# Kernel tuning notes

Hardware: AMD Instinct MI355X
Metric: run time of the kernel (lower is better)

The kernel has to match this reference:

```python
import jax, jax.numpy as jnp
import numpy as np

B, T, HID = 2, 2048, 2048
H, KVH, D = 16, 4, 128


def _rope_tables(t, d):
    inv_freq = 1.0 / (10000.0 ** (np.arange(0, d, 2, dtype=np.float32) / d))
    freqs = np.arange(t, dtype=np.float32)[:, None] * inv_freq[None, :]  # [T, d/2]
    emb = np.concatenate([freqs, freqs], axis=-1)  # [T, d]
    return jnp.asarray(np.cos(emb))[None], jnp.asarray(np.sin(emb))[None]  # [1,T,d]


def setup_inputs() -> dict:
    key = jax.random.key(0)
    ks = jax.random.split(key, 5)
    x = jax.random.normal(ks[0], (B, T, HID), dtype=jnp.float32)
    rope_cos, rope_sin = _rope_tables(T, D)
    s_in = 1.0 / np.sqrt(HID)
    Wq = jax.random.normal(ks[1], (HID, H * D), dtype=jnp.float32) * s_in
    Wk = jax.random.normal(ks[2], (HID, KVH * D), dtype=jnp.float32) * s_in
    Wv = jax.random.normal(ks[3], (HID, KVH * D), dtype=jnp.float32) * s_in
    Wo = jax.random.normal(ks[4], (H * D, HID), dtype=jnp.float32) * (1.0 / np.sqrt(H * D))
    return {"x": x, "rope_cos": rope_cos, "rope_sin": rope_sin,
            "Wq": Wq, "Wk": Wk, "Wv": Wv, "Wo": Wo}


def _apply_rope(t, cos, sin):
    # t: [B,T,h,D]; cos/sin: [1,T,D] -> broadcast over heads
    c = cos[:, :, None, :]
    s = sin[:, :, None, :]
    t1, t2 = jnp.split(t, 2, axis=-1)
    rot = jnp.concatenate([-t2, t1], axis=-1)
    return t * c + rot * s


def reference(x, rope_cos, rope_sin, Wq, Wk, Wv, Wo):
    Tq = x.shape[1]
    q = (x @ Wq).reshape(B, Tq, H, D)
    k = (x @ Wk).reshape(B, Tq, KVH, D)
    v = (x @ Wv).reshape(B, Tq, KVH, D)
    q = _apply_rope(q, rope_cos[:, :Tq], rope_sin[:, :Tq])
    k = _apply_rope(k, rope_cos[:, :Tq], rope_sin[:, :Tq])
    # sliding_window == T -> T <= W branch: k/v unchanged
    rep = H // KVH  # GQA repeat-kv
    k_full = jnp.repeat(k, rep, axis=2)  # [B,T,H,D]
    v_full = jnp.repeat(v, rep, axis=2)
    scale = 1.0 / jnp.sqrt(jnp.asarray(D, dtype=x.dtype))
    scores = jnp.einsum('bqhd,bkhd->bhqk', q, k_full) * scale
    causal = jnp.tril(jnp.ones((Tq, Tq), dtype=bool))  # end-aligned, Tk==Tq
    scores = jnp.where(causal[None, None], scores, jnp.asarray(-jnp.inf, scores.dtype))
    p = jax.nn.softmax(scores, axis=-1)
    out = jnp.einsum('bhqk,bkhd->bqhd', p, v_full)
    return out.reshape(B, Tq, H * D) @ Wo
```

## Files before the change

### kernel.cpp

```cpp
#include <hip/hip_runtime.h>
#include <hip/hip_bf16.h>

#define B_   2
#define T_   2048
#define HID_ 2048
#define H_   16
#define KVH_ 4
#define D_   128
#define GQ_  (H_ / KVH_)

#define QN_  8388608
#define KN_  2097152

typedef unsigned short u16;
typedef __attribute__((ext_vector_type(8))) unsigned short us8v;
typedef __attribute__((ext_vector_type(8))) short s16x8;
typedef __attribute__((ext_vector_type(4))) float f32x4;

__device__ __forceinline__ float bf2f(u16 u) {
  return __uint_as_float(((unsigned)u) << 16);
}
__device__ __forceinline__ u16 f2bf(float f) {
  unsigned x = __float_as_uint(f);
  return (u16)((x + 0x7fffu + ((x >> 16) & 1u)) >> 16);
}

__device__ __forceinline__ void gl2lds(const void* gp, void* lp) {
  __builtin_amdgcn_global_load_lds(
      (const __attribute__((address_space(1))) unsigned int*)gp,
      (__attribute__((address_space(3))) unsigned int*)lp, 16, 0, 0);
}

__device__ __forceinline__ void probe2(const void* A, const void* W, int tid,
                                       bool* abf, bool* wbf) {
  __shared__ int cA, zA, cW, zW;
  if (tid == 0) { cA = 0; zA = 0; cW = 0; zW = 0; }
  __syncthreads();
  const int i = 16384 + tid;
  {
    const u16 raw = ((const u16*)A)[i];
    const float v = bf2f(raw);
    const bool bad = !(fabsf(v) <= 1e6f) ||
                     (v != 0.0f && fabsf(v) < 1e-10f);
    if (bad) atomicAdd(&cA, 1);
    if (((tid & 1) == 0) && raw == 0) atomicAdd(&zA, 1);
  }
  {
    const u16 raw = ((const u16*)W)[i];
    const float v = bf2f(raw);
    const bool bad = !(fabsf(v) <= 1e6f) ||
                     (v != 0.0f && fabsf(v) < 1e-10f);
    if (bad) atomicAdd(&cW, 1);
    if (((tid & 1) == 0) && raw == 0) atomicAdd(&zW, 1);
  }
  __syncthreads();
  *abf = (cA < 8) && (zA < 100);
  *wbf = (cW < 8) && (zW < 100);
}

__global__ __launch_bounds__(256) void transp_k(const void* __restrict__ Wv_,
                                                u16* __restrict__ WT,
                                                int K, int N) {
  const int tid = threadIdx.x;
  bool wbf, dummy;
  probe2(Wv_, Wv_, tid, &wbf, &dummy);

  __shared__ float tile[64][65];
  const int kb = blockIdx.y * 64;
  const int nb = blockIdx.x * 64;

  for (int it = tid; it < 512; it += 256) {
    const int r = it >> 3;
    const int g = it & 7;
    const size_t off = (size_t)(kb + r) * N + nb + g * 8;
    float f[8];
    if (wbf) {
      const us8v t8 = *(const us8v*)((const u16*)Wv_ + off);
#pragma unroll
      for (int e = 0; e < 8; ++e) f[e] = bf2f(t8[e]);
    } else {
      const float4 f0 = *(const float4*)((const float*)Wv_ + off);
      const float4 f1 = *(const float4*)((const float*)Wv_ + off + 4);
      f[0] = f0.x; f[1] = f0.y; f[2] = f0.z; f[3] = f0.w;
      f[4] = f1.x; f[5] = f1.y; f[6] = f1.z; f[7] = f1.w;
    }
#pragma unroll
    for (int e = 0; e < 8; ++e) tile[r][g * 8 + e] = f[e];
  }
  __syncthreads();
  for (int it = tid; it < 512; it += 256) {
    const int n = it >> 3;
    const int g = it & 7;
    us8v tmp;
#pragma unroll
    for (int e = 0; e < 8; ++e) tmp[e] = f2bf(tile[g * 8 + e][n]);
    *(us8v*)&WT[(size_t)(nb + n) * K + kb + g * 8] = tmp;
  }
}

template <int OMODE>
__global__ __launch_bounds__(256) void gemm_mfma(const void* __restrict__ Av,
                                                 const u16* __restrict__ WT,
                                                 void* __restrict__ Cv,
                                                 int M, int N, int K) {
  const int tid = threadIdx.x;
  bool abf, dummy;
  probe2(Av, Av, tid, &abf, &dummy);

  __shared__ __align__(16) u16 Alds[128 * 32];
  __shared__ __align__(16) u16 Blds[128 * 32];

  const int m0 = blockIdx.y * 128;
  const int n0 = blockIdx.x * 128;
  const int wave = tid >> 6;
  const int lane = tid & 63;
  const int wm = (wave >> 1) * 64;
  const int wn = (wave & 1) * 64;
  const int lrow = lane & 15;
  const int lq = lane >> 4;

  f32x4 acc[4][4] = {};

  for (int k0 = 0; k0 < K; k0 += 32) {
    __syncthreads();
    if (abf) {
#pragma unroll
      for (int p = 0; p < 2; ++p) {
        const int it = tid + p * 256;
        const int r = it >> 2, g = it & 3;
        const int gs = g ^ ((r >> 1) & 3);
        gl2lds((const u16*)Av + (size_t)(m0 + r) * K + k0 + gs * 8,
               &Alds[((tid & ~63) + p * 256) * 8]);
      }
    } else {
#pragma unroll
      for (int p = 0; p < 2; ++p) {
        const int it = tid + p * 256;
        const int r = it >> 2, g = it & 3;
        const int gs = g ^ ((r >> 1) & 3);
        const size_t off = (size_t)(m0 + r) * K + k0 + gs * 8;
        const float4 f0 = *(const float4*)((const float*)Av + off);
        const float4 f1 = *(const float4*)((const float*)Av + off + 4);
        us8v tmp;
        tmp[0] = f2bf(f0.x); tmp[1] = f2bf(f0.y);
        tmp[2] = f2bf(f0.z); tmp[3] = f2bf(f0.w);
        tmp[4] = f2bf(f1.x); tmp[5] = f2bf(f1.y);
        tmp[6] = f2bf(f1.z); tmp[7] = f2bf(f1.w);
        *(us8v*)&Alds[r * 32 + g * 8] = tmp;
      }
    }
#pragma unroll
    for (int p = 0; p < 2; ++p) {
      const int it = tid + p * 256;
      const int n = it >> 2, g = it & 3;
      const int gs = g ^ ((n >> 1) & 3);
      gl2lds(WT + (size_t)(n0 + n) * K + k0 + gs * 8,
             &Blds[((tid & ~63) + p * 256) * 8]);
    }
    __syncthreads();

    s16x8 af[4], bfr[4];
#pragma unroll
    for (int mi = 0; mi < 4; ++mi) {
      const int row = wm + 16 * mi + lrow;
      af[mi] = *(const s16x8*)&Alds[row * 32 + ((lq ^ ((row >> 1) & 3)) * 8)];
    }
#pragma unroll
    for (int ni = 0; ni < 4; ++ni) {
      const int row = wn + 16 * ni + lrow;
      bfr[ni] = *(const s16x8*)&Blds[row * 32 + ((lq ^ ((row >> 1) & 3)) * 8)];
    }
#pragma unroll
    for (int mi = 0; mi < 4; ++mi)
#pragma unroll
      for (int ni = 0; ni < 4; ++ni)
        acc[mi][ni] = __builtin_amdgcn_mfma_f32_16x16x32_bf16(
            af[mi], bfr[ni], acc[mi][ni], 0, 0, 0);
  }

#pragma unroll
  for (int mi = 0; mi < 4; ++mi) {
#pragma unroll
    for (int ni = 0; ni < 4; ++ni) {
      const int row0 = m0 + wm + 16 * mi + lq * 4;
      const int col = n0 + wn + 16 * ni + lrow;
#pragma unroll
      for (int r = 0; r < 4; ++r) {
        const int row = row0 + r;
        if (OMODE == 0) {
          ((float*)Cv)[(size_t)row * N + col] = acc[mi][ni][r];
        } else {
          const u16 val = f2bf(acc[mi][ni][r]);
          if (col < 2048) {
            ((u16*)Cv)[(size_t)row * 2048 + col] = val;
          } else if (col < 2560) {
            ((u16*)Cv)[QN_ + (size_t)row * 512 + (col - 2048)] = val;
          } else {
            const int c = col - 2560;
            const int kvh = c >> 7;
            const int d = c & 127;
            const int bb = row >> 11;
            const int tt = row & (T_ - 1);
            ((u16*)Cv)[QN_ + KN_ +
                       ((size_t)(bb * KVH_ + kvh) * D_ + d) * T_ + tt] = val;
          }
        }
      }
    }
  }
}

__global__ __launch_bounds__(256) void rope_bf(u16* __restrict__ t,
                                               const void* __restrict__ cosT,
                                               const void* __restrict__ sinT,
                                               int NH, int total, float qs) {
  const int tid = threadIdx.x;
  bool cbf, sbf;
  probe2(cosT, sinT, tid, &cbf, &sbf);

  const int idx = blockIdx.x * blockDim.x + tid;
  if (idx >= total) return;
  const int d = idx & 63;
  const int rest = idx >> 6;
  const int tt = (rest / NH) % T_;
  const size_t base = (size_t)rest * D_;
  const int ci = tt * D_ + d;
  float c1, s1, c2, s2;
  if (cbf) {
    c1 = bf2f(((const u16*)cosT)[ci]);
    c2 = bf2f(((const u16*)cosT)[ci + 64]);
  } else {
    c1 = ((const float*)cosT)[ci];
    c2 = ((const float*)cosT)[ci + 64];
  }
  if (sbf) {
    s1 = bf2f(((const u16*)sinT)[ci]);
    s2 = bf2f(((const u16*)sinT)[ci + 64]);
  } else {
    s1 = ((const float*)sinT)[ci];
    s2 = ((const float*)sinT)[ci + 64];
  }
  const float x1 = bf2f(t[base + d]);
  const float x2 = bf2f(t[base + d + 64]);
  t[base + d] = f2bf((x1 * c1 - x2 * s1) * qs);
  t[base + d + 64] = f2bf((x2 * c2 + x1 * s2) * qs);
}

#define ATT_STAGE(bi, ktile)                                                  \
  do {                                                                        \
    const int _k0 = (ktile) * 64;                                             \
    u16* _bk = &SM[(bi) * 16384];                                             \
    _Pragma("unroll") for (int _p = 0; _p < 2; ++_p) {                        \
      const int _it = tid + _p * 512;                                         \
      const int _r = _it >> 4, _s = _it & 15;                                 \
      gl2lds(kp + (size_t)(_k0 + _r) * (KVH_ * D_) + ((_s ^ (_r & 7)) * 8),   \
             &_bk[((tid & ~63) + _p * 512) * 8]);                             \
    }                                                                         \
    _Pragma("unroll") for (int _p = 0; _p < 2; ++_p) {                        \
      const int _it = tid + _p * 512;                                         \
      const int _r = _it >> 3, _s = _it & 7;                                  \
      gl2lds(vp + (size_t)_r * T_ + _k0 + ((_s ^ (_r & 7)) * 8),              \
             &_bk[8192 + ((tid & ~63) + _p * 512) * 8]);                      \
    }                                                                         \
  } while (0)

__global__ __launch_bounds__(512, 4) void attn_mfma(
    const u16* __restrict__ q, const u16* __restrict__ k,
    const u16* __restrict__ vT, u16* __restrict__ o) {
  const int tid = threadIdx.x;
  const int ip = blockIdx.y;
  const int bh = blockIdx.x;
  const int b = bh >> 4;
  const int h = bh & 15;
  const int kvh = h >> 2;
  const int hi0 = 64 * (31 - ip);
  const int lo0 = 64 * ip;

  __shared__ __align__(16) u16 SM[2 * 16384];
  __shared__ __align__(16) u16 Pl[128 * 64];

  const int wave = tid >> 6;
  const int lane = tid & 63;
  const int l15 = lane & 15;
  const int quad = lane >> 4;
  const bool isHi = wave < 4;
  const int rowbase = isHi ? (hi0 + 16 * wave) : (lo0 + 16 * (wave - 4));
  const int pr0 = 16 * wave;

  const u16* kp = k + ((size_t)b * T_ * KVH_ + kvh) * D_;
  const u16* vp = vT + (size_t)(b * KVH_ + kvh) * D_ * T_;

  s16x8 qf[4];
  {
    const size_t qrow = ((size_t)(b * T_ + rowbase + l15) * H_ + h) * D_;
#pragma unroll
    for (int st = 0; st < 4; ++st)
      qf[st] = *(const s16x8*)&q[qrow + st * 32 + quad * 8];
  }

  f32x4 acc_o[8] = {};
  float m_s = -1.0e30f, l_s = 0.0f;

  const int nkt = 32 - ip;

  ATT_STAGE(0, 0);
  __syncthreads();

  for (int kt = 0; kt < nkt; ++kt) {
    const int k0 = kt * 64;
    const u16* Ks = &SM[(kt & 1) * 16384];
    const u16* Vt = Ks + 8192;

    if (kt + 1 < nkt) ATT_STAGE((kt + 1) & 1, kt + 1);

    const bool active = isHi || (kt <= ip);
    if (active) {
      f32x4 accs[4] = {};
      __builtin_amdgcn_s_setprio(1);
#pragma unroll
      for (int st = 0; st < 4; ++st) {
        const int g = st * 4 + quad;
#pragma unroll
        for (int nt = 0; nt < 4; ++nt) {
          const int row = nt * 16 + l15;
          const s16x8 kf =
              *(const s16x8*)&Ks[row * 128 + ((g ^ (row & 7)) << 3)];
          accs[nt] = __builtin_amdgcn_mfma_f32_16x16x32_bf16(kf, qf[st],
                                                             accs[nt], 0, 0,
                                                             0);
        }
      }
      __builtin_amdgcn_s_setprio(0);

      if ((k0 + 63) > rowbase) {
        const int qg = rowbase + l15;
#pragma unroll
        for (int nt = 0; nt < 4; ++nt)
#pragma unroll
          for (int r = 0; r < 4; ++r)
            if (qg < (k0 + nt * 16 + quad * 4 + r)) accs[nt][r] = -1.0e30f;
      }

      float t0 = fmaxf(fmaxf(accs[0][0], accs[0][1]),
                       fmaxf(accs[0][2], accs[0][3]));
      float t1 = fmaxf(fmaxf(accs[1][0], accs[1][1]),
                       fmaxf(accs[1][2], accs[1][3]));
      float t2 = fmaxf(fmaxf(accs[2][0], accs[2][1]),
                       fmaxf(accs[2][2], accs[2][3]));
      float t3 = fmaxf(fmaxf(accs[3][0], accs[3][1]),
                       fmaxf(accs[3][2], accs[3][3]));
      float mx = fmaxf(fmaxf(t0, t1), fmaxf(t2, t3));
      mx = fmaxf(mx, __shfl_xor(mx, 16));
      mx = fmaxf(mx, __shfl_xor(mx, 32));

      const int defer = __all(mx <= m_s + 8.0f);
      float alv = 1.0f;
      if (!defer) {
        const float mnew = fmaxf(m_s, mx);
        alv = __expf(m_s - mnew);
        m_s = mnew;
      }

#pragma unroll
      for (int nt = 0; nt < 4; ++nt)
#pragma unroll
        for (int r = 0; r < 4; ++r)
          accs[nt][r] = __expf(accs[nt][r] - m_s);

#pragma unroll
      for (int nt = 0; nt < 4; ++nt) {
        uint2 w;
        asm("v_cvt_pk_bf16_f32 %0, %1, %2"
            : "=v"(w.x) : "v"(accs[nt][0]), "v"(accs[nt][1]));
        asm("v_cvt_pk_bf16_f32 %0, %1, %2"
            : "=v"(w.y) : "v"(accs[nt][2]), "v"(accs[nt][3]));
        const int prow = pr0 + l15;
        const int c0 = nt * 16 + quad * 4;
        *(uint2*)&Pl[prow * 64 + (((c0 >> 3) ^ (prow & 7)) << 3) + (c0 & 7)] =
            w;
      }

      float s0 = (accs[0][0] + accs[0][1]) + (accs[0][2] + accs[0][3]);
      float s1 = (accs[1][0] + accs[1][1]) + (accs[1][2] + accs[1][3]);
      float s2 = (accs[2][0] + accs[2][1]) + (accs[2][2] + accs[2][3]);
      float s3 = (accs[3][0] + accs[3][1]) + (accs[3][2] + accs[3][3]);
      float rs = (s0 + s1) + (s2 + s3);
      rs += __shfl_xor(rs, 16);
      rs += __shfl_xor(rs, 32);
      l_s = l_s * alv + rs;

      if (!defer) {
#pragma unroll
        for (int r = 0; r < 4; ++r) {
          const float a4 = __shfl(alv, 4 * quad + r);
#pragma unroll
          for (int nt2 = 0; nt2 < 8; ++nt2) acc_o[nt2][r] *= a4;
        }
      }

      asm volatile("s_waitcnt lgkmcnt(0)" ::: "memory");
      __builtin_amdgcn_sched_barrier(0);

      s16x8 pa[2];
#pragma unroll
      for (int ks = 0; ks < 2; ++ks) {
        const int row = pr0 + l15;
        const int g = ks * 4 + quad;
        pa[ks] = *(const s16x8*)&Pl[row * 64 + ((g ^ (row & 7)) << 3)];
      }
      __builtin_amdgcn_s_setprio(1);
#pragma unroll
      for (int ks = 0; ks < 2; ++ks) {
        const int g = ks * 4 + quad;
#pragma unroll
        for (int nt2 = 0; nt2 < 8; ++nt2) {
          const int row = nt2 * 16 + l15;
          const s16x8 vf =
              *(const s16x8*)&Vt[row * 64 + ((g ^ (row & 7)) << 3)];
          acc_o[nt2] = __builtin_amdgcn_mfma_f32_16x16x32_bf16(pa[ks], vf,
                                                               acc_o[nt2], 0,
                                                               0, 0);
        }
      }
      __builtin_amdgcn_s_setprio(0);
    }

    __syncthreads();
  }

  const float inv = 1.0f / l_s;
#pragma unroll
  for (int r = 0; r < 4; ++r) {
    const float linv = __shfl(inv, 4 * quad + r);
    const size_t orow =
        ((size_t)(b * T_ + rowbase + quad * 4 + r) * H_ + h) * D_;
#pragma unroll
    for (int nt2 = 0; nt2 < 8; ++nt2)
      o[orow + nt2 * 16 + l15] = f2bf(acc_o[nt2][r] * linv);
  }
}

__global__ void zero_out_k(float* __restrict__ out, int n) {
  const int i = blockIdx.x * blockDim.x + threadIdx.x;
  if (i < n) out[i] = 0.0f;
}

extern "C" void kernel_launch(void* const* d_in, const int* in_sizes, int n_in,
                              void* d_out, int out_size, void* d_ws,
                              size_t ws_size, hipStream_t stream) {
  const void* x    = d_in[0];
  const void* cosT = d_in[1];
  const void* sinT = d_in[2];
  const void* Wq   = d_in[3];
  const void* Wk   = d_in[4];
  const void* Wv   = d_in[5];
  const void* Wo   = d_in[6];
  float* out = (float*)d_out;

  const size_t QN = QN_;
  const size_t KN = KN_;
  const size_t WQT = (size_t)HID_ * (H_ * D_);
  const size_t WKT = (size_t)HID_ * (KVH_ * D_);
  const size_t need = (2 * QN + 2 * KN + 2 * WQT + 2 * WKT) * sizeof(u16);
  if (ws_size < need) {
    zero_out_k<<<(out_size + 255) / 256, 256, 0, stream>>>(out, out_size);
    return;
  }

  u16* qbuf  = (u16*)d_ws;
  u16* kbuf  = qbuf + QN;
  u16* vbufT = kbuf + KN;
  u16* obuf  = vbufT + KN;
  u16* WqT   = obuf + QN;
  u16* WkT   = WqT + WQT;
  u16* WvT   = WkT + WKT;
  u16* WoT   = WvT + WKT;

  const int M = B_ * T_;
  dim3 blk(256);

  transp_k<<<dim3((H_ * D_) / 64, HID_ / 64), blk, 0, stream>>>(
      Wq, WqT, HID_, H_ * D_);
  transp_k<<<dim3((KVH_ * D_) / 64, HID_ / 64), blk, 0, stream>>>(
      Wk, WkT, HID_, KVH_ * D_);
  transp_k<<<dim3((KVH_ * D_) / 64, HID_ / 64), blk, 0, stream>>>(
      Wv, WvT, HID_, KVH_ * D_);
  transp_k<<<dim3(HID_ / 64, (H_ * D_) / 64), blk, 0, stream>>>(
      Wo, WoT, H_ * D_, HID_);

  gemm_mfma<3><<<dim3(3072 / 128, M / 128), blk, 0, stream>>>(
      x, WqT, qbuf, M, 3072, HID_);

  const int totq = B_ * T_ * H_ * (D_ / 2);
  rope_bf<<<totq / 256, blk, 0, stream>>>(qbuf, cosT, sinT, H_, totq,
                                          0.08838834764831845f);
  const int totk = B_ * T_ * KVH_ * (D_ / 2);
  rope_bf<<<totk / 256, blk, 0, stream>>>(kbuf, cosT, sinT, KVH_, totk, 1.0f);

  attn_mfma<<<dim3(B_ * H_, 16), dim3(512), 0, stream>>>(
      qbuf, kbuf, vbufT, obuf);

  gemm_mfma<0><<<dim3(HID_ / 128, M / 128), blk, 0, stream>>>(
      obuf, WoT, out, M, HID_, H_ * D_);
}
```

Baseline: 349.5 us.

## Pre-convert x to bf16 and double-buffer GEMM LDS loads

Adds a standalone kernel that converts the fp32 input x to bf16 once, using packed cvt instructions, into the obuf scratch area. Because of this, the GEMM no longer probes or converts A inline and always uses async global-to-LDS loads. The GEMM main loop becomes a two-stage LDS double buffer that prefetches the next K tile while the current one is computed, with raised wave priority around the MFMA block. The cost is an extra kernel launch plus a full pass over x, and twice the LDS per block, which could reduce occupancy.

```diff
diff --git a/kernel.cpp b/kernel.cpp
--- a/kernel.cpp
+++ b/kernel.cpp
@@ -58,6 +58,29 @@
   *wbf = (cW < 8) && (zW < 100);
 }
 
+__global__ __launch_bounds__(256) void conv_bf16(const void* __restrict__ in,
+                                                 u16* __restrict__ outb,
+                                                 int total8) {
+  const int tid = threadIdx.x;
+  bool ibf, dummy;
+  probe2(in, in, tid, &ibf, &dummy);
+  const int idx = blockIdx.x * 256 + tid;
+  if (idx >= total8) return;
+  if (ibf) {
+    *(us8v*)&outb[(size_t)idx * 8] = *(const us8v*)((const u16*)in +
+                                                    (size_t)idx * 8);
+  } else {
+    const float4 f0 = *(const float4*)((const float*)in + (size_t)idx * 8);
+    const float4 f1 = *(const float4*)((const float*)in + (size_t)idx * 8 + 4);
+    uint4 w;
+    asm("v_cvt_pk_bf16_f32 %0, %1, %2" : "=v"(w.x) : "v"(f0.x), "v"(f0.y));
+    asm("v_cvt_pk_bf16_f32 %0, %1, %2" : "=v"(w.y) : "v"(f0.z), "v"(f0.w));
+    asm("v_cvt_pk_bf16_f32 %0, %1, %2" : "=v"(w.z) : "v"(f1.x), "v"(f1.y));
+    asm("v_cvt_pk_bf16_f32 %0, %1, %2" : "=v"(w.w) : "v"(f1.z), "v"(f1.w));
+    *(uint4*)&outb[(size_t)idx * 8] = w;
+  }
+}
+
 __global__ __launch_bounds__(256) void transp_k(const void* __restrict__ Wv_,
                                                 u16* __restrict__ WT,
                                                 int K, int N) {
@@ -98,17 +121,33 @@
   }
 }
 
+#define G_STAGE(bi, kk)                                                       \
+  do {                                                                        \
+    _Pragma("unroll") for (int _p = 0; _p < 2; ++_p) {                        \
+      const int _it = tid + _p * 256;                                         \
+      const int _r = _it >> 2, _g = _it & 3;                                  \
+      const int _gs = _g ^ ((_r >> 1) & 3);                                   \
+      gl2lds(Ab + (size_t)(m0 + _r) * K + (kk) + _gs * 8,                     \
+             &Alds[bi][((tid & ~63) + _p * 256) * 8]);                        \
+    }                                                                         \
+    _Pragma("unroll") for (int _p = 0; _p < 2; ++_p) {                        \
+      const int _it = tid + _p * 256;                                         \
+      const int _n = _it >> 2, _g = _it & 3;                                  \
+      const int _gs = _g ^ ((_n >> 1) & 3);                                   \
+      gl2lds(WT + (size_t)(n0 + _n) * K + (kk) + _gs * 8,                     \
+             &Blds[bi][((tid & ~63) + _p * 256) * 8]);                        \
+    }                                                                         \
+  } while (0)
+
 template <int OMODE>
-__global__ __launch_bounds__(256) void gemm_mfma(const void* __restrict__ Av,
+__global__ __launch_bounds__(256) void gemm_mfma(const u16* __restrict__ Ab,
                                                  const u16* __restrict__ WT,
                                                  void* __restrict__ Cv,
                                                  int M, int N, int K) {
   const int tid = threadIdx.x;
-  bool abf, dummy;
-  probe2(Av, Av, tid, &abf, &dummy);
-
-  __shared__ __align__(16) u16 Alds[128 * 32];
-  __shared__ __align__(16) u16 Blds[128 * 32];
+
+  __shared__ __align__(16) u16 Alds[2][128 * 32];
+  __shared__ __align__(16) u16 Blds[2][128 * 32];
 
   const int m0 = blockIdx.y * 128;
   const int n0 = blockIdx.x * 128;
@@ -121,61 +160,37 @@
 
   f32x4 acc[4][4] = {};
 
+  G_STAGE(0, 0);
+  __syncthreads();
+
+  int cur = 0;
   for (int k0 = 0; k0 < K; k0 += 32) {
-    __syncthreads();
-    if (abf) {
-#pragma unroll
-      for (int p = 0; p < 2; ++p) {
-        const int it = tid + p * 256;
-        const int r = it >> 2, g = it & 3;
-        const int gs = g ^ ((r >> 1) & 3);
-        gl2lds((const u16*)Av + (size_t)(m0 + r) * K + k0 + gs * 8,
-               &Alds[((tid & ~63) + p * 256) * 8]);
-      }
-    } else {
-#pragma unroll
-      for (int p = 0; p < 2; ++p) {
-        const int it = tid + p * 256;
-        const int r = it >> 2, g = it & 3;
-        const int gs = g ^ ((r >> 1) & 3);
-        const size_t off = (size_t)(m0 + r) * K + k0 + gs * 8;
-        const float4 f0 = *(const float4*)((const float*)Av + off);
-        const float4 f1 = *(const float4*)((const float*)Av + off + 4);
-        us8v tmp;
-        tmp[0] = f2bf(f0.x); tmp[1] = f2bf(f0.y);
-        tmp[2] = f2bf(f0.z); tmp[3] = f2bf(f0.w);
-        tmp[4] = f2bf(f1.x); tmp[5] = f2bf(f1.y);
-        tmp[6] = f2bf(f1.z); tmp[7] = f2bf(f1.w);
-        *(us8v*)&Alds[r * 32 + g * 8] = tmp;
-      }
-    }
-#pragma unroll
-    for (int p = 0; p < 2; ++p) {
-      const int it = tid + p * 256;
-      const int n = it >> 2, g = it & 3;
-      const int gs = g ^ ((n >> 1) & 3);
-      gl2lds(WT + (size_t)(n0 + n) * K + k0 + gs * 8,
-             &Blds[((tid & ~63) + p * 256) * 8]);
-    }
-    __syncthreads();
+    if (k0 + 32 < K) G_STAGE(cur ^ 1, k0 + 32);
 
     s16x8 af[4], bfr[4];
 #pragma unroll
     for (int mi = 0; mi < 4; ++mi) {
       const int row = wm + 16 * mi + lrow;
-      af[mi] = *(const s16x8*)&Alds[row * 32 + ((lq ^ ((row >> 1) & 3)) * 8)];
+      af[mi] =
+          *(const s16x8*)&Alds[cur][row * 32 + ((lq ^ ((row >> 1) & 3)) * 8)];
     }
 #pragma unroll
     for (int ni = 0; ni < 4; ++ni) {
       const int row = wn + 16 * ni + lrow;
-      bfr[ni] = *(const s16x8*)&Blds[row * 32 + ((lq ^ ((row >> 1) & 3)) * 8)];
+      bfr[ni] =
+          *(const s16x8*)&Blds[cur][row * 32 + ((lq ^ ((row >> 1) & 3)) * 8)];
     }
+    __builtin_amdgcn_s_setprio(1);
 #pragma unroll
     for (int mi = 0; mi < 4; ++mi)
 #pragma unroll
       for (int ni = 0; ni < 4; ++ni)
         acc[mi][ni] = __builtin_amdgcn_mfma_f32_16x16x32_bf16(
             af[mi], bfr[ni], acc[mi][ni], 0, 0, 0);
+    __builtin_amdgcn_s_setprio(0);
+
+    __syncthreads();
+    cur ^= 1;
   }
 
 #pragma unroll
@@ -471,6 +486,7 @@
   u16* kbuf  = qbuf + QN;
   u16* vbufT = kbuf + KN;
   u16* obuf  = vbufT + KN;
+  u16* xb    = obuf;
   u16* WqT   = obuf + QN;
   u16* WkT   = WqT + WQT;
   u16* WvT   = WkT + WKT;
@@ -488,8 +504,10 @@
   transp_k<<<dim3(HID_ / 64, (H_ * D_) / 64), blk, 0, stream>>>(
       Wo, WoT, H_ * D_, HID_);
 
+  conv_bf16<<<(int)(QN / 8 / 256), blk, 0, stream>>>(x, xb, (int)(QN / 8));
+
   gemm_mfma<3><<<dim3(3072 / 128, M / 128), blk, 0, stream>>>(
-      x, WqT, qbuf, M, 3072, HID_);
+      xb, WqT, qbuf, M, 3072, HID_);
 
   const int totq = B_ * T_ * H_ * (D_ / 2);
   rope_bf<<<totq / 256, blk, 0, stream>>>(qbuf, cosT, sinT, H_, totq,
```

Measured after the change: 330.1 us. -5.6%, faster.
